# Optimization experiments

Measured on AMD Instinct MI355X. Metric: run time of the kernel, lower is better.

The kernel has to match this reference:

```python
import jax, jax.numpy as jnp
import numpy as np

H = 51  # hidden size hard-coded in the original module


def _lstm_cell(x, h, c, Wi, Wh, bi, bh):
    # torch LSTMCell: gates = x@Wi^T + bi + h@Wh^T + bh, chunks [i, f, g, o]
    g = x @ Wi.T + bi + h @ Wh.T + bh
    i, f, gg, o = jnp.split(g, 4, axis=1)
    c_new = jax.nn.sigmoid(f) * c + jax.nn.sigmoid(i) * jnp.tanh(gg)
    h_new = jax.nn.sigmoid(o) * jnp.tanh(c_new)
    return h_new, c_new


def setup_inputs() -> dict:
    key = jax.random.key(0)
    ks = jax.random.split(key, 12)
    B, T = 512, 1024
    s = 0.1
    return {
        "input": jax.random.normal(ks[0], (B, T), dtype=jnp.float32),
        "W_ih1": jax.random.normal(ks[1], (4 * H, 1), dtype=jnp.float32) * s,
        "W_hh1": jax.random.normal(ks[2], (4 * H, H), dtype=jnp.float32) * s,
        "b_ih1": jax.random.normal(ks[3], (4 * H,), dtype=jnp.float32) * s,
        "b_hh1": jax.random.normal(ks[4], (4 * H,), dtype=jnp.float32) * s,
        "W_ih2": jax.random.normal(ks[5], (4 * H, H), dtype=jnp.float32) * s,
        "W_hh2": jax.random.normal(ks[6], (4 * H, H), dtype=jnp.float32) * s,
        "b_ih2": jax.random.normal(ks[7], (4 * H,), dtype=jnp.float32) * s,
        "b_hh2": jax.random.normal(ks[8], (4 * H,), dtype=jnp.float32) * s,
        "W_lin": jax.random.normal(ks[9], (1, H), dtype=jnp.float32) * s,
        "b_lin": jax.random.normal(ks[10], (1,), dtype=jnp.float32) * s,
        "future": 64,
    }


def reference(input, W_ih1, W_hh1, b_ih1, b_hh1, W_ih2, W_hh2, b_ih2, b_hh2,
              W_lin, b_lin, future):
    B = input.shape[0]
    h1 = jnp.zeros((B, H), dtype=input.dtype)
    c1 = jnp.zeros((B, H), dtype=input.dtype)
    h2 = jnp.zeros((B, H), dtype=input.dtype)
    c2 = jnp.zeros((B, H), dtype=input.dtype)

    def step(carry, x_t):
        h1, c1, h2, c2 = carry
        h1, c1 = _lstm_cell(x_t, h1, c1, W_ih1, W_hh1, b_ih1, b_hh1)
        h2, c2 = _lstm_cell(h1, h2, c2, W_ih2, W_hh2, b_ih2, b_hh2)
        out = h2 @ W_lin.T + b_lin  # [B, 1]
        return (h1, c1, h2, c2), out

    xs = input.T[:, :, None]  # [T, B, 1] timestep-major
    carry, outs = jax.lax.scan(step, (h1, c1, h2, c2), xs)
    last_out = outs[-1]  # [B, 1]

    def fstep(carry, _):
        h1, c1, h2, c2, out = carry
        h1, c1 = _lstm_cell(out, h1, c1, W_ih1, W_hh1, b_ih1, b_hh1)
        h2, c2 = _lstm_cell(h1, h2, c2, W_ih2, W_hh2, b_ih2, b_hh2)
        out = h2 @ W_lin.T + b_lin
        return (h1, c1, h2, c2, out), out

    _, fouts = jax.lax.scan(fstep, (*carry, last_out), None, length=future)
    all_outs = jnp.concatenate([outs, fouts], axis=0)  # [T+future, B, 1]
    return all_outs[:, :, 0].T  # [B, T+future]
```

## Files before the change

### kernel.cpp

```cpp
#include <hip/hip_runtime.h>
#include <math.h>

#define HID 51
#define TMAIN 1024
#define FUT 64
#define TT (TMAIN + FUT)

typedef float v2f __attribute__((ext_vector_type(2)));

__device__ __forceinline__ float fast_sigmoid(float x) {
  return 1.0f / (1.0f + __expf(-x));
}
__device__ __forceinline__ float fast_tanh(float x) {
  return 1.0f - 2.0f / (__expf(2.0f * x) + 1.0f);
}

__device__ __forceinline__ void dot2x(const float* hA, const float* hB,
                                      const v2f (&w2)[2][25],
                                      const float (&w50)[2],
                                      float (&aA)[2], float (&aB)[2]) {
  const float4* a4 = reinterpret_cast<const float4*>(hA);
  const float4* b4 = reinterpret_cast<const float4*>(hB);
  v2f sA0 = {0.f, 0.f}, sA1 = {0.f, 0.f};
  v2f sB0 = {0.f, 0.f}, sB1 = {0.f, 0.f};
#pragma unroll
  for (int q = 0; q < 12; ++q) {
    float4 av = a4[q];
    float4 bv = b4[q];
    v2f alo = {av.x, av.y}, ahi = {av.z, av.w};
    v2f blo = {bv.x, bv.y}, bhi = {bv.z, bv.w};
    sA0 = __builtin_elementwise_fma(alo, w2[0][2 * q + 0], sA0);
    sB0 = __builtin_elementwise_fma(blo, w2[0][2 * q + 0], sB0);
    sA1 = __builtin_elementwise_fma(alo, w2[1][2 * q + 0], sA1);
    sB1 = __builtin_elementwise_fma(blo, w2[1][2 * q + 0], sB1);
    sA0 = __builtin_elementwise_fma(ahi, w2[0][2 * q + 1], sA0);
    sB0 = __builtin_elementwise_fma(bhi, w2[0][2 * q + 1], sB0);
    sA1 = __builtin_elementwise_fma(ahi, w2[1][2 * q + 1], sA1);
    sB1 = __builtin_elementwise_fma(bhi, w2[1][2 * q + 1], sB1);
  }
  float4 at = a4[12];
  float4 bt = b4[12];
  v2f alo = {at.x, at.y}, blo = {bt.x, bt.y};
  sA0 = __builtin_elementwise_fma(alo, w2[0][24], sA0);
  sB0 = __builtin_elementwise_fma(blo, w2[0][24], sB0);
  sA1 = __builtin_elementwise_fma(alo, w2[1][24], sA1);
  sB1 = __builtin_elementwise_fma(blo, w2[1][24], sB1);
  aA[0] = fmaf(at.z, w50[0], aA[0] + sA0.x + sA0.y);
  aB[0] = fmaf(bt.z, w50[0], aB[0] + sB0.x + sB0.y);
  aA[1] = fmaf(at.z, w50[1], aA[1] + sA1.x + sA1.y);
  aB[1] = fmaf(bt.z, w50[1], aB[1] + sB1.x + sB1.y);
}

__global__ __launch_bounds__(384, 2)
void lstm2_persistent(const float* __restrict__ input,
                      const float* __restrict__ Wi1,
                      const float* __restrict__ Wh1,
                      const float* __restrict__ bi1,
                      const float* __restrict__ bh1,
                      const float* __restrict__ Wi2,
                      const float* __restrict__ Wh2,
                      const float* __restrict__ bi2,
                      const float* __restrict__ bh2,
                      const float* __restrict__ Wlin,
                      const float* __restrict__ blin,
                      float* __restrict__ out) {
  __shared__ __align__(16) float lds_x[2][TMAIN];
  __shared__ __align__(16) float lds_h1[2][2][64];
  __shared__ __align__(16) float lds_h2[2][2][64];
  __shared__ __align__(16) float lds_pi[2][2][4][64];
  __shared__ __align__(16) float lds_outbuf[2][128];
  __shared__ float lds_lin[2][2][2];

  const int tid = threadIdx.x;
  const int s0 = blockIdx.x * 2;
  const int wid = tid >> 6;
  const int lane = tid & 63;
  const int half = lane >> 5;
  const int l5 = lane & 31;
  const int base = (wid & 1) * 26;
  const int nu = (wid & 1) ? 25 : 26;
  const bool act = l5 < nu;
  const int u = base + (act ? l5 : 0);
  const int g0 = half * 2;
  const int seq23 = (wid == 3) ? 1 : 0;

  for (int i = tid; i < TMAIN; i += 384) {
    lds_x[0][i] = input[s0 * TMAIN + i];
    lds_x[1][i] = input[(s0 + 1) * TMAIN + i];
  }
  if (tid < 64) {
#pragma unroll
    for (int p = 0; p < 2; ++p) {
      lds_h1[0][p][tid] = 0.0f;
      lds_h1[1][p][tid] = 0.0f;
      lds_h2[0][p][tid] = 0.0f;
      lds_h2[1][p][tid] = 0.0f;
    }
  }

  v2f w2[2][25];
  float w50[2];
  float bias[2] = {0.f, 0.f};
  float wi1g[2] = {0.f, 0.f};
  float wlin_u = 0.0f;
  float wlin_lane = 0.0f;
  float cA = 0.0f, cB = 0.0f;

  const float* Wsel = (wid < 2) ? Wh1 : ((wid < 4) ? Wi2 : Wh2);
#pragma unroll
  for (int g = 0; g < 2; ++g) {
    const float* row = Wsel + ((g0 + g) * HID + u) * HID;
#pragma unroll
    for (int p = 0; p < 25; ++p) {
      v2f t;
      t.x = row[2 * p + 0];
      t.y = row[2 * p + 1];
      w2[g][p] = t;
    }
    w50[g] = row[50];
  }
  if (wid < 2) {
#pragma unroll
    for (int g = 0; g < 2; ++g) {
      bias[g] = bi1[(g0 + g) * HID + u] + bh1[(g0 + g) * HID + u];
      wi1g[g] = Wi1[(g0 + g) * HID + u];
    }
  } else if (wid < 4) {
#pragma unroll
    for (int g = 0; g < 2; ++g)
      bias[g] = bi2[(g0 + g) * HID + u] + bh2[(g0 + g) * HID + u];
    wlin_lane = (lane < HID) ? Wlin[lane] : 0.0f;
  } else {
    wlin_u = Wlin[u];
  }
  const float blin_s = blin[0];

#pragma unroll
  for (int g = 0; g < 2; ++g) {
#pragma unroll
    for (int p = 0; p < 25; ++p) asm volatile("" : "+v"(w2[g][p]));
    asm volatile("" : "+v"(w50[g]), "+v"(bias[g]), "+v"(wi1g[g]));
  }
  asm volatile("" : "+v"(wlin_u), "+v"(wlin_lane));

  __syncthreads();

  for (int k = 0; k <= TMAIN + 2; ++k) {
    if (wid < 2) {
      if (k < TMAIN) {
        float xA = lds_x[0][k], xB = lds_x[1][k];
        float aA[2], aB[2];
#pragma unroll
        for (int g = 0; g < 2; ++g) {
          aA[g] = fmaf(xA, wi1g[g], bias[g]);
          aB[g] = fmaf(xB, wi1g[g], bias[g]);
        }
        dot2x(lds_h1[0][k & 1], lds_h1[1][k & 1], w2, w50, aA, aB);
        float pA0 = __shfl_xor(aA[0], 32), pA1 = __shfl_xor(aA[1], 32);
        float pB0 = __shfl_xor(aB[0], 32), pB1 = __shfl_xor(aB[1], 32);
        float giA = half ? pA0 : aA[0], gfA = half ? pA1 : aA[1];
        float ggA = half ? aA[0] : pA0, goA = half ? aA[1] : pA1;
        float giB = half ? pB0 : aB[0], gfB = half ? pB1 : aB[1];
        float ggB = half ? aB[0] : pB0, goB = half ? aB[1] : pB1;
        cA = fast_sigmoid(gfA) * cA + fast_sigmoid(giA) * fast_tanh(ggA);
        cB = fast_sigmoid(gfB) * cB + fast_sigmoid(giB) * fast_tanh(ggB);
        float hA = fast_sigmoid(goA) * fast_tanh(cA);
        float hB = fast_sigmoid(goB) * fast_tanh(cB);
        if (act && half == 0) {
          lds_h1[0][(k + 1) & 1][u] = hA;
          lds_h1[1][(k + 1) & 1][u] = hB;
        }
      }
    } else if (wid < 4) {
      if (k >= 1 && k <= TMAIN) {
        float aA[2] = {bias[0], bias[1]}, aB[2] = {bias[0], bias[1]};
        dot2x(lds_h1[0][k & 1], lds_h1[1][k & 1], w2, w50, aA, aB);
        if (act) {
          const int pm = (k - 1) & 1;
          lds_pi[pm][0][g0 + 0][u] = aA[0];
          lds_pi[pm][0][g0 + 1][u] = aA[1];
          lds_pi[pm][1][g0 + 0][u] = aB[0];
          lds_pi[pm][1][g0 + 1][u] = aB[1];
        }
      }
      if (k >= 3) {
        const int m = k - 3;
        float hv = lds_h2[seq23][m & 1][lane];
        float val = wlin_lane * hv;
#pragma unroll
        for (int off = 32; off >= 1; off >>= 1) val += __shfl_xor(val, off);
        if (lane == 0) lds_outbuf[seq23][m & 127] = val + blin_s;
        if ((m & 63) == 63) {
          const int idx = (m - 63) + lane;
          out[(s0 + seq23) * TT + idx] = lds_outbuf[seq23][idx & 127];
        }
      }
    } else {
      if (k >= 2 && k <= TMAIN + 1) {
        const int m2 = k - 2;
        float aA[2], aB[2];
        aA[0] = lds_pi[m2 & 1][0][g0 + 0][u];
        aA[1] = lds_pi[m2 & 1][0][g0 + 1][u];
        aB[0] = lds_pi[m2 & 1][1][g0 + 0][u];
        aB[1] = lds_pi[m2 & 1][1][g0 + 1][u];
        dot2x(lds_h2[0][(m2 - 1) & 1], lds_h2[1][(m2 - 1) & 1], w2, w50, aA,
              aB);
        float pA0 = __shfl_xor(aA[0], 32), pA1 = __shfl_xor(aA[1], 32);
        float pB0 = __shfl_xor(aB[0], 32), pB1 = __shfl_xor(aB[1], 32);
        float giA = half ? pA0 : aA[0], gfA = half ? pA1 : aA[1];
        float ggA = half ? aA[0] : pA0, goA = half ? aA[1] : pA1;
        float giB = half ? pB0 : aB[0], gfB = half ? pB1 : aB[1];
        float ggB = half ? aB[0] : pB0, goB = half ? aB[1] : pB1;
        cA = fast_sigmoid(gfA) * cA + fast_sigmoid(giA) * fast_tanh(ggA);
        cB = fast_sigmoid(gfB) * cB + fast_sigmoid(giB) * fast_tanh(ggB);
        float hA = fast_sigmoid(goA) * fast_tanh(cA);
        float hB = fast_sigmoid(goB) * fast_tanh(cB);
        if (act && half == 0) {
          lds_h2[0][m2 & 1][u] = hA;
          lds_h2[1][m2 & 1][u] = hB;
        }
      }
    }
    __syncthreads();
  }

  for (int t = TMAIN; t < TT; ++t) {
    float phA[2] = {0.f, 0.f}, phB[2] = {0.f, 0.f};
    if (wid < 2) {
      float oA, oB;
      if (t == TMAIN) {
        oA = lds_outbuf[0][127];
        oB = lds_outbuf[1][127];
      } else {
        oA = lds_lin[(t - 1) & 1][0][0] + lds_lin[(t - 1) & 1][0][1] + blin_s;
        oB = lds_lin[(t - 1) & 1][1][0] + lds_lin[(t - 1) & 1][1][1] + blin_s;
        if (lane == 0) {
          if (wid == 0) lds_outbuf[0][(t - 1) & 127] = oA;
          else          lds_outbuf[1][(t - 1) & 127] = oB;
        }
      }
      float aA[2], aB[2];
#pragma unroll
      for (int g = 0; g < 2; ++g) {
        aA[g] = fmaf(oA, wi1g[g], bias[g]);
        aB[g] = fmaf(oB, wi1g[g], bias[g]);
      }
      dot2x(lds_h1[0][t & 1], lds_h1[1][t & 1], w2, w50, aA, aB);
      float pA0 = __shfl_xor(aA[0], 32), pA1 = __shfl_xor(aA[1], 32);
      float pB0 = __shfl_xor(aB[0], 32), pB1 = __shfl_xor(aB[1], 32);
      float giA = half ? pA0 : aA[0], gfA = half ? pA1 : aA[1];
      float ggA = half ? aA[0] : pA0, goA = half ? aA[1] : pA1;
      float giB = half ? pB0 : aB[0], gfB = half ? pB1 : aB[1];
      float ggB = half ? aB[0] : pB0, goB = half ? aB[1] : pB1;
      cA = fast_sigmoid(gfA) * cA + fast_sigmoid(giA) * fast_tanh(ggA);
      cB = fast_sigmoid(gfB) * cB + fast_sigmoid(giB) * fast_tanh(ggB);
      float hA = fast_sigmoid(goA) * fast_tanh(cA);
      float hB = fast_sigmoid(goB) * fast_tanh(cB);
      if (act && half == 0) {
        lds_h1[0][(t + 1) & 1][u] = hA;
        lds_h1[1][(t + 1) & 1][u] = hB;
      }
    } else if (wid >= 4) {
      dot2x(lds_h2[0][(t - 1) & 1], lds_h2[1][(t - 1) & 1], w2, w50, phA, phB);
    }
    __syncthreads();
    if (wid >= 2 && wid < 4) {
      float aA[2] = {bias[0], bias[1]}, aB[2] = {bias[0], bias[1]};
      dot2x(lds_h1[0][(t + 1) & 1], lds_h1[1][(t + 1) & 1], w2, w50, aA, aB);
      if (act) {
        const int pm = t & 1;
        lds_pi[pm][0][g0 + 0][u] = aA[0];
        lds_pi[pm][0][g0 + 1][u] = aA[1];
        lds_pi[pm][1][g0 + 0][u] = aB[0];
        lds_pi[pm][1][g0 + 1][u] = aB[1];
      }
    }
    __syncthreads();
    if (wid >= 4) {
      float aA[2], aB[2];
      aA[0] = lds_pi[t & 1][0][g0 + 0][u] + phA[0];
      aA[1] = lds_pi[t & 1][0][g0 + 1][u] + phA[1];
      aB[0] = lds_pi[t & 1][1][g0 + 0][u] + phB[0];
      aB[1] = lds_pi[t & 1][1][g0 + 1][u] + phB[1];
      float pA0 = __shfl_xor(aA[0], 32), pA1 = __shfl_xor(aA[1], 32);
      float pB0 = __shfl_xor(aB[0], 32), pB1 = __shfl_xor(aB[1], 32);
      float giA = half ? pA0 : aA[0], gfA = half ? pA1 : aA[1];
      float ggA = half ? aA[0] : pA0, goA = half ? aA[1] : pA1;
      float giB = half ? pB0 : aB[0], gfB = half ? pB1 : aB[1];
      float ggB = half ? aB[0] : pB0, goB = half ? aB[1] : pB1;
      cA = fast_sigmoid(gfA) * cA + fast_sigmoid(giA) * fast_tanh(ggA);
      cB = fast_sigmoid(gfB) * cB + fast_sigmoid(giB) * fast_tanh(ggB);
      float hA = fast_sigmoid(goA) * fast_tanh(cA);
      float hB = fast_sigmoid(goB) * fast_tanh(cB);
      float val = 0.0f;
      if (act) {
        if (half == 0) {
          lds_h2[0][t & 1][u] = hA;
          val = wlin_u * hA;
        } else {
          lds_h2[1][t & 1][u] = hB;
          val = wlin_u * hB;
        }
      }
#pragma unroll
      for (int off = 16; off >= 1; off >>= 1) val += __shfl_xor(val, off);
      if (lane == 0) lds_lin[t & 1][0][wid - 4] = val;
      if (lane == 32) lds_lin[t & 1][1][wid - 4] = val;
    }
    __syncthreads();
  }

  if (wid < 2 && lane == 0) {
    float o = lds_lin[(TT - 1) & 1][wid][0] + lds_lin[(TT - 1) & 1][wid][1] +
              blin_s;
    lds_outbuf[wid][(TT - 1) & 127] = o;
  }
  __syncthreads();
  if (wid >= 2 && wid < 4) {
    const int tt = TMAIN + lane;
    out[(s0 + seq23) * TT + tt] = lds_outbuf[seq23][tt & 127];
  }
}

extern "C" void kernel_launch(void* const* d_in, const int* in_sizes, int n_in,
                              void* d_out, int out_size, void* d_ws,
                              size_t ws_size, hipStream_t stream) {
  const float* input = (const float*)d_in[0];
  const float* Wi1 = (const float*)d_in[1];
  const float* Wh1 = (const float*)d_in[2];
  const float* bi1 = (const float*)d_in[3];
  const float* bh1 = (const float*)d_in[4];
  const float* Wi2 = (const float*)d_in[5];
  const float* Wh2 = (const float*)d_in[6];
  const float* bi2 = (const float*)d_in[7];
  const float* bh2 = (const float*)d_in[8];
  const float* Wlin = (const float*)d_in[9];
  const float* blin = (const float*)d_in[10];
  float* out = (float*)d_out;

  const int B = in_sizes[0] / TMAIN;
  lstm2_persistent<<<B / 2, 384, 0, stream>>>(input, Wi1, Wh1, bi1, bh1, Wi2,
                                              Wh2, bi2, bh2, Wlin, blin, out);
}
```

Measured before the change: 1.511 ms.

## Split layer-2 input projection across four extra waves and batch output projection

```diff
diff --git a/kernel.cpp b/kernel.cpp
--- a/kernel.cpp
+++ b/kernel.cpp
@@ -5,6 +5,8 @@
 #define TMAIN 1024
 #define FUT 64
 #define TT (TMAIN + FUT)
+#define RING 128
+#define RPAD 68
 
 typedef float v2f __attribute__((ext_vector_type(2)));
 
@@ -51,7 +53,29 @@
   aB[1] = fmaf(bt.z, w50[1], aB[1] + sB1.x + sB1.y);
 }
 
-__global__ __launch_bounds__(384, 2)
+__device__ __forceinline__ void dotH(const float* hA, const float* hB,
+                                     const v2f (&w)[2][13],
+                                     float (&aA)[2], float (&aB)[2]) {
+  const float2* a2 = reinterpret_cast<const float2*>(hA);
+  const float2* b2 = reinterpret_cast<const float2*>(hB);
+  v2f sA0 = {0.f, 0.f}, sA1 = {0.f, 0.f};
+  v2f sB0 = {0.f, 0.f}, sB1 = {0.f, 0.f};
+#pragma unroll
+  for (int p = 0; p < 13; ++p) {
+    float2 av = a2[p], bv = b2[p];
+    v2f a = {av.x, av.y}, b = {bv.x, bv.y};
+    sA0 = __builtin_elementwise_fma(a, w[0][p], sA0);
+    sB0 = __builtin_elementwise_fma(b, w[0][p], sB0);
+    sA1 = __builtin_elementwise_fma(a, w[1][p], sA1);
+    sB1 = __builtin_elementwise_fma(b, w[1][p], sB1);
+  }
+  aA[0] = sA0.x + sA0.y;
+  aB[0] = sB0.x + sB0.y;
+  aA[1] = sA1.x + sA1.y;
+  aB[1] = sB1.x + sB1.y;
+}
+
+__global__ __launch_bounds__(512, 2)
 void lstm2_persistent(const float* __restrict__ input,
                       const float* __restrict__ Wi1,
                       const float* __restrict__ Wh1,
@@ -66,10 +90,13 @@
                       float* __restrict__ out) {
   __shared__ __align__(16) float lds_x[2][TMAIN];
   __shared__ __align__(16) float lds_h1[2][2][64];
-  __shared__ __align__(16) float lds_h2[2][2][64];
-  __shared__ __align__(16) float lds_pi[2][2][4][64];
-  __shared__ __align__(16) float lds_outbuf[2][128];
+  __shared__ __align__(16) float lds_piK1[2][2][4][64];
+  __shared__ __align__(16) float lds_piK2[2][2][4][64];
+  __shared__ __align__(16) float lds_h2h[2][RING][RPAD];
+  __shared__ __align__(16) float lds_wlin[64];
+  __shared__ __align__(16) float lds_outbuf[2][64];
   __shared__ float lds_lin[2][2][2];
+  __shared__ float lds_fb[2];
 
   const int tid = threadIdx.x;
   const int s0 = blockIdx.x * 2;
@@ -82,66 +109,94 @@
   const bool act = l5 < nu;
   const int u = base + (act ? l5 : 0);
   const int g0 = half * 2;
-  const int seq23 = (wid == 3) ? 1 : 0;
-
-  for (int i = tid; i < TMAIN; i += 384) {
+  const int koff = (wid >= 6) ? 0 : 26;
+
+  for (int i = tid; i < TMAIN; i += 512) {
     lds_x[0][i] = input[s0 * TMAIN + i];
     lds_x[1][i] = input[(s0 + 1) * TMAIN + i];
   }
   if (tid < 64) {
-#pragma unroll
-    for (int p = 0; p < 2; ++p) {
-      lds_h1[0][p][tid] = 0.0f;
-      lds_h1[1][p][tid] = 0.0f;
-      lds_h2[0][p][tid] = 0.0f;
-      lds_h2[1][p][tid] = 0.0f;
-    }
-  }
-
-  v2f w2[2][25];
-  float w50[2];
+    lds_h1[0][0][tid] = 0.0f;
+    lds_h1[0][1][tid] = 0.0f;
+    lds_h1[1][0][tid] = 0.0f;
+    lds_h1[1][1][tid] = 0.0f;
+    lds_wlin[tid] = (tid < HID) ? Wlin[tid] : 0.0f;
+  }
+  if (tid < 128) lds_h2h[tid >> 6][RING - 1][tid & 63] = 0.0f;
+
+  v2f w2f[2][25];
+  float w50f[2] = {0.f, 0.f};
+  v2f w2h[2][13];
   float bias[2] = {0.f, 0.f};
   float wi1g[2] = {0.f, 0.f};
   float wlin_u = 0.0f;
-  float wlin_lane = 0.0f;
   float cA = 0.0f, cB = 0.0f;
 
-  const float* Wsel = (wid < 2) ? Wh1 : ((wid < 4) ? Wi2 : Wh2);
-#pragma unroll
-  for (int g = 0; g < 2; ++g) {
-    const float* row = Wsel + ((g0 + g) * HID + u) * HID;
-#pragma unroll
-    for (int p = 0; p < 25; ++p) {
-      v2f t;
-      t.x = row[2 * p + 0];
-      t.y = row[2 * p + 1];
-      w2[g][p] = t;
-    }
-    w50[g] = row[50];
-  }
-  if (wid < 2) {
+  if (wid < 4) {
+    const float* Wsel = (wid < 2) ? Wh1 : Wh2;
 #pragma unroll
     for (int g = 0; g < 2; ++g) {
-      bias[g] = bi1[(g0 + g) * HID + u] + bh1[(g0 + g) * HID + u];
-      wi1g[g] = Wi1[(g0 + g) * HID + u];
-    }
-  } else if (wid < 4) {
+      const float* row = Wsel + ((g0 + g) * HID + u) * HID;
+#pragma unroll
+      for (int p = 0; p < 25; ++p) {
+        v2f t;
+        t.x = row[2 * p + 0];
+        t.y = row[2 * p + 1];
+        w2f[g][p] = t;
+      }
+      w50f[g] = row[50];
+    }
+    if (wid < 2) {
+#pragma unroll
+      for (int g = 0; g < 2; ++g) {
+        bias[g] = bi1[(g0 + g) * HID + u] + bh1[(g0 + g) * HID + u];
+        wi1g[g] = Wi1[(g0 + g) * HID + u];
+      }
+    } else {
+#pragma unroll
+      for (int g = 0; g < 2; ++g)
+        bias[g] = bi2[(g0 + g) * HID + u] + bh2[(g0 + g) * HID + u];
+      wlin_u = Wlin[u];
+    }
+#pragma unroll
+    for (int g = 0; g < 2; ++g) {
+#pragma unroll
+      for (int p = 0; p < 25; ++p) asm volatile("" : "+v"(w2f[g][p]));
+      asm volatile("" : "+v"(w50f[g]), "+v"(bias[g]), "+v"(wi1g[g]));
+    }
+    asm volatile("" : "+v"(wlin_u));
+  } else {
+#pragma unroll
+    for (int g = 0; g < 2; ++g) {
+      const float* row = Wi2 + ((g0 + g) * HID + u) * HID + koff;
+      if (koff == 0) {
+#pragma unroll
+        for (int p = 0; p < 13; ++p) {
+          v2f t;
+          t.x = row[2 * p + 0];
+          t.y = row[2 * p + 1];
+          w2h[g][p] = t;
+        }
+      } else {
+#pragma unroll
+        for (int p = 0; p < 12; ++p) {
+          v2f t;
+          t.x = row[2 * p + 0];
+          t.y = row[2 * p + 1];
+          w2h[g][p] = t;
+        }
+        v2f t;
+        t.x = row[24];
+        t.y = 0.0f;
+        w2h[g][12] = t;
+      }
+    }
 #pragma unroll
     for (int g = 0; g < 2; ++g)
-      bias[g] = bi2[(g0 + g) * HID + u] + bh2[(g0 + g) * HID + u];
-    wlin_lane = (lane < HID) ? Wlin[lane] : 0.0f;
-  } else {
-    wlin_u = Wlin[u];
+#pragma unroll
+      for (int p = 0; p < 13; ++p) asm volatile("" : "+v"(w2h[g][p]));
   }
   const float blin_s = blin[0];
-
-#pragma unroll
-  for (int g = 0; g < 2; ++g) {
-#pragma unroll
-    for (int p = 0; p < 25; ++p) asm volatile("" : "+v"(w2[g][p]));
-    asm volatile("" : "+v"(w50[g]), "+v"(bias[g]), "+v"(wi1g[g]));
-  }
-  asm volatile("" : "+v"(wlin_u), "+v"(wlin_lane));
 
   __syncthreads();
 
@@ -155,7 +210,7 @@
           aA[g] = fmaf(xA, wi1g[g], bias[g]);
           aB[g] = fmaf(xB, wi1g[g], bias[g]);
         }
-        dot2x(lds_h1[0][k & 1], lds_h1[1][k & 1], w2, w50, aA, aB);
+        dot2x(lds_h1[0][k & 1], lds_h1[1][k & 1], w2f, w50f, aA, aB);
         float pA0 = __shfl_xor(aA[0], 32), pA1 = __shfl_xor(aA[1], 32);
         float pB0 = __shfl_xor(aB[0], 32), pB1 = __shfl_xor(aB[1], 32);
         float giA = half ? pA0 : aA[0], gfA = half ? pA1 : aA[1];
@@ -172,39 +227,16 @@
         }
       }
     } else if (wid < 4) {
-      if (k >= 1 && k <= TMAIN) {
-        float aA[2] = {bias[0], bias[1]}, aB[2] = {bias[0], bias[1]};
-        dot2x(lds_h1[0][k & 1], lds_h1[1][k & 1], w2, w50, aA, aB);
-        if (act) {
-          const int pm = (k - 1) & 1;
-          lds_pi[pm][0][g0 + 0][u] = aA[0];
-          lds_pi[pm][0][g0 + 1][u] = aA[1];
-          lds_pi[pm][1][g0 + 0][u] = aB[0];
-          lds_pi[pm][1][g0 + 1][u] = aB[1];
-        }
-      }
-      if (k >= 3) {
-        const int m = k - 3;
-        float hv = lds_h2[seq23][m & 1][lane];
-        float val = wlin_lane * hv;
-#pragma unroll
-        for (int off = 32; off >= 1; off >>= 1) val += __shfl_xor(val, off);
-        if (lane == 0) lds_outbuf[seq23][m & 127] = val + blin_s;
-        if ((m & 63) == 63) {
-          const int idx = (m - 63) + lane;
-          out[(s0 + seq23) * TT + idx] = lds_outbuf[seq23][idx & 127];
-        }
-      }
-    } else {
       if (k >= 2 && k <= TMAIN + 1) {
         const int m2 = k - 2;
+        const int pm = m2 & 1;
         float aA[2], aB[2];
-        aA[0] = lds_pi[m2 & 1][0][g0 + 0][u];
-        aA[1] = lds_pi[m2 & 1][0][g0 + 1][u];
-        aB[0] = lds_pi[m2 & 1][1][g0 + 0][u];
-        aB[1] = lds_pi[m2 & 1][1][g0 + 1][u];
-        dot2x(lds_h2[0][(m2 - 1) & 1], lds_h2[1][(m2 - 1) & 1], w2, w50, aA,
-              aB);
+        aA[0] = bias[0] + lds_piK1[pm][0][g0 + 0][u] + lds_piK2[pm][0][g0 + 0][u];
+        aA[1] = bias[1] + lds_piK1[pm][0][g0 + 1][u] + lds_piK2[pm][0][g0 + 1][u];
+        aB[0] = bias[0] + lds_piK1[pm][1][g0 + 0][u] + lds_piK2[pm][1][g0 + 0][u];
+        aB[1] = bias[1] + lds_piK1[pm][1][g0 + 1][u] + lds_piK2[pm][1][g0 + 1][u];
+        dot2x(&lds_h2h[0][(m2 - 1) & (RING - 1)][0],
+              &lds_h2h[1][(m2 - 1) & (RING - 1)][0], w2f, w50f, aA, aB);
         float pA0 = __shfl_xor(aA[0], 32), pA1 = __shfl_xor(aA[1], 32);
         float pB0 = __shfl_xor(aB[0], 32), pB1 = __shfl_xor(aB[1], 32);
         float giA = half ? pA0 : aA[0], gfA = half ? pA1 : aA[1];
@@ -216,9 +248,46 @@
         float hA = fast_sigmoid(goA) * fast_tanh(cA);
         float hB = fast_sigmoid(goB) * fast_tanh(cB);
         if (act && half == 0) {
-          lds_h2[0][m2 & 1][u] = hA;
-          lds_h2[1][m2 & 1][u] = hB;
-        }
+          lds_h2h[0][m2 & (RING - 1)][u] = hA;
+          lds_h2h[1][m2 & (RING - 1)][u] = hB;
+        }
+      }
+    } else {
+      if (k >= 1 && k <= TMAIN) {
+        float aA[2], aB[2];
+        dotH(&lds_h1[0][k & 1][koff], &lds_h1[1][k & 1][koff], w2h, aA, aB);
+        const int pm = (k - 1) & 1;
+        if (act) {
+          if (wid >= 6) {
+            lds_piK1[pm][0][g0 + 0][u] = aA[0];
+            lds_piK1[pm][0][g0 + 1][u] = aA[1];
+            lds_piK1[pm][1][g0 + 0][u] = aB[0];
+            lds_piK1[pm][1][g0 + 1][u] = aB[1];
+          } else {
+            lds_piK2[pm][0][g0 + 0][u] = aA[0];
+            lds_piK2[pm][0][g0 + 1][u] = aA[1];
+            lds_piK2[pm][1][g0 + 0][u] = aB[0];
+            lds_piK2[pm][1][g0 + 1][u] = aB[1];
+          }
+        }
+      }
+      if (wid < 6 && k >= 66 && ((k - 66) & 63) == 0) {
+        const int c = k - 66;
+        const int seq = wid - 4;
+        const int m = c + lane;
+        const float* r = &lds_h2h[seq][m & (RING - 1)][0];
+        float o0 = 0.f, o1 = 0.f;
+#pragma unroll
+        for (int j = 0; j < 48; j += 2) {
+          o0 = fmaf(lds_wlin[j], r[j], o0);
+          o1 = fmaf(lds_wlin[j + 1], r[j + 1], o1);
+        }
+        o0 = fmaf(lds_wlin[48], r[48], o0);
+        o1 = fmaf(lds_wlin[49], r[49], o1);
+        o0 = fmaf(lds_wlin[50], r[50], o0);
+        float o = o0 + o1 + blin_s;
+        out[(s0 + seq) * TT + m] = o;
+        if (m == TMAIN - 1) lds_fb[seq] = o;
       }
     }
     __syncthreads();
@@ -229,14 +298,14 @@
     if (wid < 2) {
       float oA, oB;
       if (t == TMAIN) {
-        oA = lds_outbuf[0][127];
-        oB = lds_outbuf[1][127];
+        oA = lds_fb[0];
+        oB = lds_fb[1];
       } else {
         oA = lds_lin[(t - 1) & 1][0][0] + lds_lin[(t - 1) & 1][0][1] + blin_s;
         oB = lds_lin[(t - 1) & 1][1][0] + lds_lin[(t - 1) & 1][1][1] + blin_s;
         if (lane == 0) {
-          if (wid == 0) lds_outbuf[0][(t - 1) & 127] = oA;
-          else          lds_outbuf[1][(t - 1) & 127] = oB;
+          if (wid == 0) lds_outbuf[0][t - 1 - TMAIN] = oA;
+          else          lds_outbuf[1][t - 1 - TMAIN] = oB;
         }
       }
       float aA[2], aB[2];
@@ -245,7 +314,7 @@
         aA[g] = fmaf(oA, wi1g[g], bias[g]);
         aB[g] = fmaf(oB, wi1g[g], bias[g]);
       }
-      dot2x(lds_h1[0][t & 1], lds_h1[1][t & 1], w2, w50, aA, aB);
+      dot2x(lds_h1[0][t & 1], lds_h1[1][t & 1], w2f, w50f, aA, aB);
       float pA0 = __shfl_xor(aA[0], 32), pA1 = __shfl_xor(aA[1], 32);
       float pB0 = __shfl_xor(aB[0], 32), pB1 = __shfl_xor(aB[1], 32);
       float giA = half ? pA0 : aA[0], gfA = half ? pA1 : aA[1];
@@ -260,28 +329,38 @@
         lds_h1[0][(t + 1) & 1][u] = hA;
         lds_h1[1][(t + 1) & 1][u] = hB;
       }
-    } else if (wid >= 4) {
-      dot2x(lds_h2[0][(t - 1) & 1], lds_h2[1][(t - 1) & 1], w2, w50, phA, phB);
-    }
-    __syncthreads();
-    if (wid >= 2 && wid < 4) {
-      float aA[2] = {bias[0], bias[1]}, aB[2] = {bias[0], bias[1]};
-      dot2x(lds_h1[0][(t + 1) & 1], lds_h1[1][(t + 1) & 1], w2, w50, aA, aB);
-      if (act) {
-        const int pm = t & 1;
-        lds_pi[pm][0][g0 + 0][u] = aA[0];
-        lds_pi[pm][0][g0 + 1][u] = aA[1];
-        lds_pi[pm][1][g0 + 0][u] = aB[0];
-        lds_pi[pm][1][g0 + 1][u] = aB[1];
-      }
+    } else if (wid < 4) {
+      dot2x(&lds_h2h[0][(t - 1) & (RING - 1)][0],
+            &lds_h2h[1][(t - 1) & (RING - 1)][0], w2f, w50f, phA, phB);
     }
     __syncthreads();
     if (wid >= 4) {
       float aA[2], aB[2];
-      aA[0] = lds_pi[t & 1][0][g0 + 0][u] + phA[0];
-      aA[1] = lds_pi[t & 1][0][g0 + 1][u] + phA[1];
-      aB[0] = lds_pi[t & 1][1][g0 + 0][u] + phB[0];
-      aB[1] = lds_pi[t & 1][1][g0 + 1][u] + phB[1];
+      dotH(&lds_h1[0][(t + 1) & 1][koff], &lds_h1[1][(t + 1) & 1][koff], w2h,
+           aA, aB);
+      const int pm = t & 1;
+      if (act) {
+        if (wid >= 6) {
+          lds_piK1[pm][0][g0 + 0][u] = aA[0];
+          lds_piK1[pm][0][g0 + 1][u] = aA[1];
+          lds_piK1[pm][1][g0 + 0][u] = aB[0];
+          lds_piK1[pm][1][g0 + 1][u] = aB[1];
+        } else {
+          lds_piK2[pm][0][g0 + 0][u] = aA[0];
+          lds_piK2[pm][0][g0 + 1][u] = aA[1];
+          lds_piK2[pm][1][g0 + 0][u] = aB[0];
+          lds_piK2[pm][1][g0 + 1][u] = aB[1];
+        }
+      }
+    }
+    __syncthreads();
+    if (wid >= 2 && wid < 4) {
+      const int pm = t & 1;
+      float aA[2], aB[2];
+      aA[0] = bias[0] + lds_piK1[pm][0][g0 + 0][u] + lds_piK2[pm][0][g0 + 0][u] + phA[0];
+      aA[1] = bias[1] + lds_piK1[pm][0][g0 + 1][u] + lds_piK2[pm][0][g0 + 1][u] + phA[1];
+      aB[0] = bias[0] + lds_piK1[pm][1][g0 + 0][u] + lds_piK2[pm][1][g0 + 0][u] + phB[0];
+      aB[1] = bias[1] + lds_piK1[pm][1][g0 + 1][u] + lds_piK2[pm][1][g0 + 1][u] + phB[1];
       float pA0 = __shfl_xor(aA[0], 32), pA1 = __shfl_xor(aA[1], 32);
       float pB0 = __shfl_xor(aB[0], 32), pB1 = __shfl_xor(aB[1], 32);
       float giA = half ? pA0 : aA[0], gfA = half ? pA1 : aA[1];
@@ -295,17 +374,17 @@
       float val = 0.0f;
       if (act) {
         if (half == 0) {
-          lds_h2[0][t & 1][u] = hA;
+          lds_h2h[0][t & (RING - 1)][u] = hA;
           val = wlin_u * hA;
         } else {
-          lds_h2[1][t & 1][u] = hB;
+          lds_h2h[1][t & (RING - 1)][u] = hB;
           val = wlin_u * hB;
         }
       }
 #pragma unroll
       for (int off = 16; off >= 1; off >>= 1) val += __shfl_xor(val, off);
-      if (lane == 0) lds_lin[t & 1][0][wid - 4] = val;
-      if (lane == 32) lds_lin[t & 1][1][wid - 4] = val;
+      if (lane == 0) lds_lin[t & 1][0][wid - 2] = val;
+      if (lane == 32) lds_lin[t & 1][1][wid - 2] = val;
     }
     __syncthreads();
   }
@@ -313,12 +392,12 @@
   if (wid < 2 && lane == 0) {
     float o = lds_lin[(TT - 1) & 1][wid][0] + lds_lin[(TT - 1) & 1][wid][1] +
               blin_s;
-    lds_outbuf[wid][(TT - 1) & 127] = o;
+    lds_outbuf[wid][63] = o;
   }
   __syncthreads();
-  if (wid >= 2 && wid < 4) {
-    const int tt = TMAIN + lane;
-    out[(s0 + seq23) * TT + tt] = lds_outbuf[seq23][tt & 127];
+  if (wid == 4 || wid == 5) {
+    const int seq = wid - 4;
+    out[(s0 + seq) * TT + TMAIN + lane] = lds_outbuf[seq][lane];
   }
 }
 
@@ -339,6 +418,6 @@
   float* out = (float*)d_out;
 
   const int B = in_sizes[0] / TMAIN;
-  lstm2_persistent<<<B / 2, 384, 0, stream>>>(input, Wi1, Wh1, bi1, bh1, Wi2,
+  lstm2_persistent<<<B / 2, 512, 0, stream>>>(input, Wi1, Wh1, bi1, bh1, Wi2,
                                               Wh2, bi2, bh2, Wlin, blin, out);
 }
```

Result: faster. 1.394 ms (-7.8%).
